# Kernel optimization log

Hardware: AMD Instinct MI355X
Metric: run time of the kernel (lower is better)

Reference implementation:

```python
import jax, jax.numpy as jnp
import numpy as np

N_NODES = 100000
N_EDGES = 1600000
IN_CH = 128
TYPE_EMB = 32
OUT_CH = 128
N_REL = 8
N_BASES = 8
N_NTYPES = 8
FEAT = IN_CH + TYPE_EMB  # 160, RGCNConv input dim after concat


def setup_inputs() -> dict:
    key = jax.random.key(0)
    ks = jax.random.split(key, 9)
    x = jax.random.normal(ks[0], (N_NODES, IN_CH), dtype=jnp.float32)
    node_type_ids = jax.random.randint(ks[1], (N_NODES,), 0, N_NTYPES)
    edge_index = jax.random.randint(ks[2], (2, N_EDGES), 0, N_NODES)
    edge_type = jax.random.randint(ks[3], (N_EDGES,), 0, N_REL)
    emb_table = jax.random.normal(ks[4], (N_NTYPES, TYPE_EMB), dtype=jnp.float32)
    bases = jax.random.normal(ks[5], (N_BASES, FEAT, OUT_CH), dtype=jnp.float32) * (1.0 / np.sqrt(FEAT))
    comp = jax.random.normal(ks[6], (N_REL, N_BASES), dtype=jnp.float32) * (1.0 / np.sqrt(N_BASES))
    root_w = jax.random.normal(ks[7], (FEAT, OUT_CH), dtype=jnp.float32) * (1.0 / np.sqrt(FEAT))
    bias = jnp.zeros((OUT_CH,), dtype=jnp.float32)
    return {"x": x, "node_type_ids": node_type_ids, "edge_index": edge_index,
            "edge_type": edge_type, "emb_table": emb_table, "bases": bases,
            "comp": comp, "root_w": root_w, "bias": bias}


def reference(x, node_type_ids, edge_index, edge_type, emb_table, bases, comp, root_w, bias):
    N = x.shape[0]
    # node-type embedding lookup + concat
    h = jnp.concatenate([x, emb_table[node_type_ids]], axis=1)  # [N, FEAT]
    # basis decomposition: per-relation weights [R, FEAT, OUT]
    weight = jnp.einsum('rb,bio->rio', comp, bases)
    src, dst = edge_index[0], edge_index[1]
    h_src = h[src]  # [E, FEAT] -- dominant gather
    # root/self transform + bias
    out = h @ root_w + bias
    # PyG RGCNConv default aggr='mean': per-relation mean over incoming edges, summed across relations
    for r in range(weight.shape[0]):
        m = (edge_type == r).astype(h.dtype)  # [E]
        s = jax.ops.segment_sum(h_src * m[:, None], dst, num_segments=N)  # [N, FEAT]
        c = jax.ops.segment_sum(m, dst, num_segments=N)                    # [N]
        mean_r = s / jnp.maximum(c, 1.0)[:, None]
        out = out + mean_r @ weight[r]
    # dropout is identity in eval mode
    return jax.nn.relu(out)
```

## Files before the change

### kernel.cpp

```cpp
#include <hip/hip_runtime.h>

#define NN 100000
#define NE 1600000
#define INC 128
#define TE 32
#define OC 128
#define NR 8
#define NBASES 8
#define FT 160
#define KP 168
#define KW 160
#define TN 32
#define NBKT 3125
#define NCH 128
#define EPB 12500
#define CAP 896

typedef float f32x4 __attribute__((ext_vector_type(4)));
typedef float f32x2 __attribute__((ext_vector_type(2)));
typedef __bf16 bf16x8 __attribute__((ext_vector_type(8)));

__device__ __forceinline__ unsigned f2bf1(float f) {
    unsigned u = __float_as_uint(f);
    return (u + 0x7fffu + ((u >> 16) & 1u)) >> 16;
}

__device__ __forceinline__ float bflo(unsigned u) { return __uint_as_float(u << 16); }
__device__ __forceinline__ float bfhi(unsigned u) { return __uint_as_float(u & 0xFFFF0000u); }

__device__ __forceinline__ unsigned cvtpk(float a, float b) {
    unsigned r;
    asm("v_cvt_pk_bf16_f32 %0, %1, %2" : "=v"(r) : "v"(a), "v"(b));
    return r;
}

__device__ __forceinline__ int bscan_excl(int v, int* tmp) {
    int tid = threadIdx.x;
    tmp[tid] = v; __syncthreads();
#pragma unroll
    for (int d = 1; d < 256; d <<= 1) {
        int t = (tid >= d) ? tmp[tid - d] : 0;
        __syncthreads();
        tmp[tid] += t;
        __syncthreads();
    }
    return tmp[tid] - v;
}

__global__ __launch_bounds__(256) void k_prep(
    const float* __restrict__ x, const int* __restrict__ nt,
    const float* __restrict__ emb, const float* __restrict__ comp,
    const float* __restrict__ bases, const float* __restrict__ rootw,
    const int* __restrict__ ei,
    unsigned short* __restrict__ h, unsigned short* __restrict__ Wt,
    int* __restrict__ ghist, int* __restrict__ total) {
    __shared__ int hist[NBKT];
    int tid = threadIdx.x;
    int b = blockIdx.x;
    if (b < NCH) {
        for (int j = tid; j < NBKT; j += 256) hist[j] = 0;
        __syncthreads();
        int e0 = b * EPB;
#pragma unroll
        for (int k = 0; k < 49; k++) {
            int i = k * 256 + tid;
            if (i < EPB) atomicAdd(&hist[ei[NE + e0 + i] >> 5], 1);
        }
        __syncthreads();
        int* g = ghist + (size_t)b * NBKT;
        for (int j = tid; j < NBKT; j += 256) {
            int v = hist[j];
            g[j] = v;
            if (v) atomicAdd(&total[j], v);
        }
        return;
    }
    int idx = (b - NCH) * 256 + tid;
    if (idx < 9 * 128 * KW) {
        int ridx = idx / (128 * KW);
        int rem  = idx % (128 * KW);
        int o = rem / KW;
        int k = rem % KW;
        float v = 0.f;
        if (k < 128) {
            if (ridx < NR) {
#pragma unroll
                for (int bb = 0; bb < NBASES; bb++)
                    v += comp[ridx * NBASES + bb] * bases[(bb * FT + k) * OC + o];
            } else {
                v = rootw[k * OC + o];
            }
        } else if (k < 136) {
            int t = k - 128;
            if (ridx < NR) {
#pragma unroll
                for (int bb = 0; bb < NBASES; bb++) {
                    float cb = comp[ridx * NBASES + bb], s2 = 0.f;
                    for (int k2 = 0; k2 < TE; k2++)
                        s2 += emb[t * TE + k2] * bases[(bb * FT + 128 + k2) * OC + o];
                    v += cb * s2;
                }
            } else {
                for (int k2 = 0; k2 < TE; k2++)
                    v += emb[t * TE + k2] * rootw[(128 + k2) * OC + o];
            }
        }
        Wt[idx] = (unsigned short)f2bf1(v);
    }
    if (idx < NN * 16) {
        int n = idx / 16, c = idx % 16;
        const float* p = x + (size_t)n * INC + c * 8;
        f32x4 v0 = *(const f32x4*)p, v1 = *(const f32x4*)(p + 4);
        uint4 o;
        o.x = f2bf1(v0.x) | (f2bf1(v0.y) << 16);
        o.y = f2bf1(v0.z) | (f2bf1(v0.w) << 16);
        o.z = f2bf1(v1.x) | (f2bf1(v1.y) << 16);
        o.w = f2bf1(v1.z) | (f2bf1(v1.w) << 16);
        *(uint4*)(h + (size_t)n * INC + c * 8) = o;
    }
}

__global__ __launch_bounds__(256) void k_scanoff(const int* __restrict__ total,
                                                 int* __restrict__ ghist,
                                                 int* __restrict__ bstart) {
    __shared__ int tot[NBKT];
    __shared__ int tmp[256];
    int tid = threadIdx.x;
    for (int j = tid; j < NBKT; j += 256) tot[j] = total[j];
    __syncthreads();
    int i0 = tid * 13, s = 0;
    int loc[13];
#pragma unroll
    for (int i = 0; i < 13; i++) {
        int j = i0 + i;
        loc[i] = (j < NBKT) ? tot[j] : 0;
        s += loc[i];
    }
    int run = bscan_excl(s, tmp);
#pragma unroll
    for (int i = 0; i < 13; i++) {
        int j = i0 + i;
        if (j < NBKT) tot[j] = run;
        run += loc[i];
    }
    __syncthreads();
    if (blockIdx.x == 0) {
        for (int j = tid; j < NBKT; j += 256) bstart[j] = tot[j];
        if (tid == 0) bstart[NBKT] = NE;
    }
    int j = blockIdx.x * 256 + tid;
    if (j < NBKT) {
        int run2 = tot[j];
#pragma unroll 4
        for (int b = 0; b < NCH; b++) {
            int v = ghist[(size_t)b * NBKT + j];
            ghist[(size_t)b * NBKT + j] = run2;
            run2 += v;
        }
    }
}

__global__ __launch_bounds__(256) void k_scatter(const int* __restrict__ ei, const int* __restrict__ et,
                                                 const int* __restrict__ nt,
                                                 const int* __restrict__ ghist, unsigned* __restrict__ slots) {
    __shared__ int cur[NBKT];
    int tid = threadIdx.x, b = blockIdx.x;
    for (int j = tid; j < NBKT; j += 256) cur[j] = ghist[(size_t)b * NBKT + j];
    __syncthreads();
    int e0 = b * EPB;
#pragma unroll
    for (int kk = 0; kk < 52; kk += 4) {
        int sv[4], dv[4], rv[4], tv[4];
#pragma unroll
        for (int u = 0; u < 4; u++) {
            int i = (kk + u) * 256 + tid;
            int e = e0 + ((i < EPB) ? i : 0);
            sv[u] = ei[e]; dv[u] = ei[NE + e]; rv[u] = et[e];
            if (i >= EPB) dv[u] = -1;
        }
#pragma unroll
        for (int u = 0; u < 4; u++) tv[u] = nt[sv[u]];
#pragma unroll
        for (int u = 0; u < 4; u++) {
            if (dv[u] >= 0) {
                int pos = atomicAdd(&cur[dv[u] >> 5], 1);
                slots[pos] = (unsigned)sv[u] | ((unsigned)rv[u] << 17)
                           | ((unsigned)(dv[u] & 31) << 20) | ((unsigned)tv[u] << 25);
            }
        }
    }
}

__global__ __launch_bounds__(256, 6) void k_mega(
    const unsigned short* __restrict__ h, const int* __restrict__ nt,
    const float* __restrict__ bias,
    const unsigned short* __restrict__ Wt, const int* __restrict__ bstart,
    const unsigned* __restrict__ slots, float* __restrict__ out) {
    __shared__ unsigned short featmem[2][TN * KP];
    __shared__ unsigned sl[CAP];
    __shared__ unsigned pkl[256];

    const int tid = threadIdx.x;
    const int lane = tid & 63;
    const int wave = tid >> 6;
    const int j = blockIdx.x;
    const int n0 = j * TN;

    unsigned* sl_in = reinterpret_cast<unsigned*>(&featmem[0][0]);
    int* hist = reinterpret_cast<int*>(&featmem[0][0]) + CAP;
    int* tmp  = reinterpret_cast<int*>(&featmem[0][0]) + CAP + 256;

    int s0 = bstart[j];
    int m = bstart[j + 1] - s0; if (m > CAP) m = CAP;
    for (int i = tid; i < m; i += 256) sl_in[i] = slots[s0 + i];
    hist[tid] = 0;
    __syncthreads();
    for (int i = tid; i < m; i += 256) {
        unsigned v = sl_in[i];
        atomicAdd(&hist[((v >> 17) & 7u) * 32u + ((v >> 20) & 31u)], 1);
    }
    __syncthreads();
    int v0 = hist[tid];
    int ex = bscan_excl(v0, tmp);
    pkl[tid] = (unsigned)ex | ((unsigned)v0 << 16);
    hist[tid] = ex;
    __syncthreads();
    for (int i = tid; i < m; i += 256) {
        unsigned v = sl_in[i];
        int p = atomicAdd(&hist[((v >> 17) & 7u) * 32u + ((v >> 20) & 31u)], 1);
        sl[p] = (v & 0x1FFFFu) | (((v >> 25) & 7u) << 17);
    }
    __syncthreads();

    for (int i = tid; i < TN * 20; i += 256) {
        int nl = i / 20, c = i % 20, n = n0 + nl;
        uint4 v;
        if (c < 16) {
            v = *reinterpret_cast<const uint4*>(h + (size_t)n * INC + c * 8);
        } else if (c == 16) {
            int t = nt[n];
            v.x = (t == 0 ? 0x3F80u : 0u) | (t == 1 ? 0x3F800000u : 0u);
            v.y = (t == 2 ? 0x3F80u : 0u) | (t == 3 ? 0x3F800000u : 0u);
            v.z = (t == 4 ? 0x3F80u : 0u) | (t == 5 ? 0x3F800000u : 0u);
            v.w = (t == 6 ? 0x3F80u : 0u) | (t == 7 ? 0x3F800000u : 0u);
        } else {
            v = (uint4){0u, 0u, 0u, 0u};
        }
        *reinterpret_cast<uint4*>(&featmem[0][nl * KP + c * 8]) = v;
    }

    f32x4 acc[4];
#pragma unroll
    for (int t = 0; t < 4; t++) acc[t] = (f32x4){0.f, 0.f, 0.f, 0.f};

    auto mfma_pass = [&](int ridx, const unsigned short* fm) {
        const unsigned short* fA = fm + (lane & 15) * KP + ((lane >> 4) * 8);
        const unsigned short* gB = Wt + (size_t)ridx * 128 * KW
                                   + (wave * 32 + (lane & 15)) * KW + ((lane >> 4) * 8);
#pragma unroll
        for (int kc = 0; kc < 5; kc++) {
            bf16x8 a0 = *reinterpret_cast<const bf16x8*>(fA + 0 * 16 * KP + kc * 32);
            bf16x8 a1 = *reinterpret_cast<const bf16x8*>(fA + 1 * 16 * KP + kc * 32);
#pragma unroll
            for (int ct = 0; ct < 2; ct++) {
                bf16x8 b = *reinterpret_cast<const bf16x8*>(gB + ct * 16 * KW + kc * 32);
                acc[0 * 2 + ct] = __builtin_amdgcn_mfma_f32_16x16x32_bf16(a0, b, acc[0 * 2 + ct], 0, 0, 0);
                acc[1 * 2 + ct] = __builtin_amdgcn_mfma_f32_16x16x32_bf16(a1, b, acc[1 * 2 + ct], 0, 0, 0);
            }
        }
    };

    const int g = tid >> 4, l = tid & 15;
    const unsigned* hw = reinterpret_cast<const unsigned*>(h);

    auto agg_pass = [&](int r, unsigned short* fm) {
        int b0 = r * 32 + 2 * g;
        unsigned pk0 = pkl[b0], pk1 = pkl[b0 + 1];
        int sbeg = (int)(pk0 & 0xffffu);
        int e1 = (int)(pk1 & 0xffffu);
        int send = e1 + (int)(pk1 >> 16);
        f32x2 sa[4];
#pragma unroll
        for (int i = 0; i < 4; i++) sa[i] = (f32x2){0.f, 0.f};
        f32x2 cnt2 = (f32x2){0.f, 0.f};
        float run = 0.f;
        for (int e = sbeg; e < send; e += 4) {
            uint4 wv[4]; unsigned tpk = 0;
#pragma unroll
            for (int u = 0; u < 4; u++) {
                int eu = e + u; if (eu >= send) eu = send - 1;
                unsigned v = sl[eu];
                wv[u] = *reinterpret_cast<const uint4*>(hw + (size_t)(v & 0x1FFFFu) * 64 + 4 * l);
                tpk |= ((v >> 17) & 7u) << (3 * u);
            }
#pragma unroll
            for (int u = 0; u < 4; u++) {
                if (e + u < send) {
                    sa[0] += (f32x2){bflo(wv[u].x), bfhi(wv[u].x)};
                    sa[1] += (f32x2){bflo(wv[u].y), bfhi(wv[u].y)};
                    sa[2] += (f32x2){bflo(wv[u].z), bfhi(wv[u].z)};
                    sa[3] += (f32x2){bflo(wv[u].w), bfhi(wv[u].w)};
                    int tt = (int)((tpk >> (3 * u)) & 7u);
                    cnt2.x += (tt == 2 * l)     ? 1.f : 0.f;
                    cnt2.y += (tt == 2 * l + 1) ? 1.f : 0.f;
                    run += 1.f;
                    int nx = e + u + 1;
                    if (nx == e1 || nx == send) {
                        int q = (e + u >= e1) ? 1 : 0;
                        float inv = __builtin_amdgcn_rcpf(run);
                        f32x2 m0 = sa[0] * inv, m1 = sa[1] * inv, m2 = sa[2] * inv,
                              m3 = sa[3] * inv, fr = cnt2 * inv;
                        unsigned* fp = reinterpret_cast<unsigned*>(fm + (2 * g + q) * KP);
                        uint4 o;
                        o.x = cvtpk(m0.x, m0.y);
                        o.y = cvtpk(m1.x, m1.y);
                        o.z = cvtpk(m2.x, m2.y);
                        o.w = cvtpk(m3.x, m3.y);
                        *reinterpret_cast<uint4*>(fp + 4 * l) = o;
                        fp[64 + l] = cvtpk(fr.x, fr.y);
#pragma unroll
                        for (int i = 0; i < 4; i++) sa[i] = (f32x2){0.f, 0.f};
                        cnt2 = (f32x2){0.f, 0.f};
                        run = 0.f;
                    }
                }
            }
        }
#pragma unroll
        for (int q = 0; q < 2; q++) {
            if ((pkl[b0 + q] >> 16) == 0u) {
                unsigned* fp = reinterpret_cast<unsigned*>(fm + (2 * g + q) * KP);
                *reinterpret_cast<uint4*>(fp + 4 * l) = (uint4){0u, 0u, 0u, 0u};
                fp[64 + l] = 0u;
            }
        }
    };

    __syncthreads();
    int prev = 8;
    for (int r = 0; r < NR; r++) {
        agg_pass(r, &featmem[(r + 1) & 1][0]);
        mfma_pass(prev, &featmem[r & 1][0]);
        prev = r;
        __syncthreads();
    }
    mfma_pass(7, &featmem[0][0]);

    const int rq = lane >> 4;
#pragma unroll
    for (int ct = 0; ct < 2; ct++) {
        int col = wave * 32 + ct * 16 + (lane & 15);
        float bv = bias[col];
#pragma unroll
        for (int rt = 0; rt < 2; rt++) {
#pragma unroll
            for (int i = 0; i < 4; i++) {
                int n = n0 + rt * 16 + rq * 4 + i;
                float v = acc[rt * 2 + ct][i] + bv;
                out[(size_t)n * OC + col] = v > 0.f ? v : 0.f;
            }
        }
    }
}

extern "C" void kernel_launch(void* const* d_in, const int* in_sizes, int n_in,
                              void* d_out, int out_size, void* d_ws, size_t ws_size,
                              hipStream_t stream) {
    const float* x     = (const float*)d_in[0];
    const int*   ntype = (const int*)d_in[1];
    const int*   ei    = (const int*)d_in[2];
    const int*   et    = (const int*)d_in[3];
    const float* emb   = (const float*)d_in[4];
    const float* bases = (const float*)d_in[5];
    const float* comp  = (const float*)d_in[6];
    const float* rootw = (const float*)d_in[7];
    const float* bias  = (const float*)d_in[8];
    float* out = (float*)d_out;

    char* ws = (char*)d_ws;
    unsigned short* Wt     = (unsigned short*)(ws);
    unsigned short* h      = (unsigned short*)(ws + 368640);
    int*            ghist  = (int*)(ws + 25968640);
    int*            total  = (int*)(ws + 27568640);
    int*            bstart = (int*)(ws + 27581184);
    unsigned*       slots  = (unsigned*)(ws + 27593728);

    hipMemsetAsync(total, 0, NBKT * sizeof(int), stream);
    k_prep   <<<NCH + 6250, 256, 0, stream>>>(x, ntype, emb, comp, bases, rootw, ei, h, Wt, ghist, total);
    k_scanoff<<<13,   256, 0, stream>>>(total, ghist, bstart);
    k_scatter<<<NCH,  256, 0, stream>>>(ei, et, ntype, ghist, slots);
    k_mega   <<<NBKT, 256, 0, stream>>>(h, ntype, bias, Wt, bstart, slots, out);
}
```

Baseline: 369.6 us.

## Double edge-chunk count, batch histogram loads, split gather into two half-row loads

Doubles the number of edge chunks used by the histogram and scatter kernels, halving edges per block so more blocks run in parallel; the per-chunk histogram is enlarged and the workspace offsets shift to fit it. The histogram loop now loads four destination indices before issuing the shared atomics, exposing memory-level parallelism. In the aggregation pass each lane now reads two 8-byte pieces of a gathered row (first and second half) instead of one 16-byte piece, so the 16 lanes of a group touch contiguous 128-byte halves. The trade-off is more global histogram traffic and a longer serial prefix loop over chunks in the scan kernel.

After: 339.8 us. 8.1% less time.

```diff
diff --git a/kernel.cpp b/kernel.cpp
--- a/kernel.cpp
+++ b/kernel.cpp
@@ -12,8 +12,8 @@
 #define KW 160
 #define TN 32
 #define NBKT 3125
-#define NCH 128
-#define EPB 12500
+#define NCH 256
+#define EPB 6250
 #define CAP 896
 
 typedef float f32x4 __attribute__((ext_vector_type(4)));
@@ -62,9 +62,16 @@
         __syncthreads();
         int e0 = b * EPB;
 #pragma unroll
-        for (int k = 0; k < 49; k++) {
-            int i = k * 256 + tid;
-            if (i < EPB) atomicAdd(&hist[ei[NE + e0 + i] >> 5], 1);
+        for (int kk = 0; kk < 28; kk += 4) {
+            int dv[4];
+#pragma unroll
+            for (int u = 0; u < 4; u++) {
+                int i = (kk + u) * 256 + tid;
+                dv[u] = (i < EPB) ? ei[NE + e0 + i] : -1;
+            }
+#pragma unroll
+            for (int u = 0; u < 4; u++)
+                if (dv[u] >= 0) atomicAdd(&hist[dv[u] >> 5], 1);
         }
         __syncthreads();
         int* g = ghist + (size_t)b * NBKT;
@@ -151,7 +158,7 @@
     int j = blockIdx.x * 256 + tid;
     if (j < NBKT) {
         int run2 = tot[j];
-#pragma unroll 4
+#pragma unroll 8
         for (int b = 0; b < NCH; b++) {
             int v = ghist[(size_t)b * NBKT + j];
             ghist[(size_t)b * NBKT + j] = run2;
@@ -169,7 +176,7 @@
     __syncthreads();
     int e0 = b * EPB;
 #pragma unroll
-    for (int kk = 0; kk < 52; kk += 4) {
+    for (int kk = 0; kk < 28; kk += 4) {
         int sv[4], dv[4], rv[4], tv[4];
 #pragma unroll
         for (int u = 0; u < 4; u++) {
@@ -285,21 +292,23 @@
         f32x2 cnt2 = (f32x2){0.f, 0.f};
         float run = 0.f;
         for (int e = sbeg; e < send; e += 4) {
-            uint4 wv[4]; unsigned tpk = 0;
+            uint2 wa[4], wb[4]; unsigned tpk = 0;
 #pragma unroll
             for (int u = 0; u < 4; u++) {
                 int eu = e + u; if (eu >= send) eu = send - 1;
                 unsigned v = sl[eu];
-                wv[u] = *reinterpret_cast<const uint4*>(hw + (size_t)(v & 0x1FFFFu) * 64 + 4 * l);
+                const unsigned* hp = hw + (size_t)(v & 0x1FFFFu) * 64 + 2 * l;
+                wa[u] = *reinterpret_cast<const uint2*>(hp);
+                wb[u] = *reinterpret_cast<const uint2*>(hp + 32);
                 tpk |= ((v >> 17) & 7u) << (3 * u);
             }
 #pragma unroll
             for (int u = 0; u < 4; u++) {
                 if (e + u < send) {
-                    sa[0] += (f32x2){bflo(wv[u].x), bfhi(wv[u].x)};
-                    sa[1] += (f32x2){bflo(wv[u].y), bfhi(wv[u].y)};
-                    sa[2] += (f32x2){bflo(wv[u].z), bfhi(wv[u].z)};
-                    sa[3] += (f32x2){bflo(wv[u].w), bfhi(wv[u].w)};
+                    sa[0] += (f32x2){bflo(wa[u].x), bfhi(wa[u].x)};
+                    sa[1] += (f32x2){bflo(wa[u].y), bfhi(wa[u].y)};
+                    sa[2] += (f32x2){bflo(wb[u].x), bfhi(wb[u].x)};
+                    sa[3] += (f32x2){bflo(wb[u].y), bfhi(wb[u].y)};
                     int tt = (int)((tpk >> (3 * u)) & 7u);
                     cnt2.x += (tt == 2 * l)     ? 1.f : 0.f;
                     cnt2.y += (tt == 2 * l + 1) ? 1.f : 0.f;
@@ -311,12 +320,13 @@
                         f32x2 m0 = sa[0] * inv, m1 = sa[1] * inv, m2 = sa[2] * inv,
                               m3 = sa[3] * inv, fr = cnt2 * inv;
                         unsigned* fp = reinterpret_cast<unsigned*>(fm + (2 * g + q) * KP);
-                        uint4 o;
-                        o.x = cvtpk(m0.x, m0.y);
-                        o.y = cvtpk(m1.x, m1.y);
-                        o.z = cvtpk(m2.x, m2.y);
-                        o.w = cvtpk(m3.x, m3.y);
-                        *reinterpret_cast<uint4*>(fp + 4 * l) = o;
+                        uint2 oa, ob;
+                        oa.x = cvtpk(m0.x, m0.y);
+                        oa.y = cvtpk(m1.x, m1.y);
+                        ob.x = cvtpk(m2.x, m2.y);
+                        ob.y = cvtpk(m3.x, m3.y);
+                        *reinterpret_cast<uint2*>(fp + 2 * l) = oa;
+                        *reinterpret_cast<uint2*>(fp + 32 + 2 * l) = ob;
                         fp[64 + l] = cvtpk(fr.x, fr.y);
 #pragma unroll
                         for (int i = 0; i < 4; i++) sa[i] = (f32x2){0.f, 0.f};
@@ -330,7 +340,8 @@
         for (int q = 0; q < 2; q++) {
             if ((pkl[b0 + q] >> 16) == 0u) {
                 unsigned* fp = reinterpret_cast<unsigned*>(fm + (2 * g + q) * KP);
-                *reinterpret_cast<uint4*>(fp + 4 * l) = (uint4){0u, 0u, 0u, 0u};
+                *reinterpret_cast<uint2*>(fp + 2 * l) = (uint2){0u, 0u};
+                *reinterpret_cast<uint2*>(fp + 32 + 2 * l) = (uint2){0u, 0u};
                 fp[64 + l] = 0u;
             }
         }
@@ -381,9 +392,9 @@
     unsigned short* Wt     = (unsigned short*)(ws);
     unsigned short* h      = (unsigned short*)(ws + 368640);
     int*            ghist  = (int*)(ws + 25968640);
-    int*            total  = (int*)(ws + 27568640);
-    int*            bstart = (int*)(ws + 27581184);
-    unsigned*       slots  = (unsigned*)(ws + 27593728);
+    int*            total  = (int*)(ws + 29168640);
+    int*            bstart = (int*)(ws + 29181184);
+    unsigned*       slots  = (unsigned*)(ws + 29193728);
 
     hipMemsetAsync(total, 0, NBKT * sizeof(int), stream);
     k_prep   <<<NCH + 6250, 256, 0, stream>>>(x, ntype, emb, comp, bases, rootw, ei, h, Wt, ghist, total);
```
